# Kernel tuning notes

Measured on AMD Instinct MI355X. Metric: run time of the kernel, lower is better.

The kernel has to match this reference:

```python
import jax, jax.numpy as jnp
import numpy as np

B, S, IN, H, D, M, OUT, TOPK = 4, 256, 256, 512, 128, 100000, 256, 3
EPS = 1e-12  # F.normalize eps


def _l2norm(x):
    n = jnp.sqrt(jnp.sum(x * x, axis=-1, keepdims=True))
    return x / jnp.maximum(n, EPS)


def setup_inputs() -> dict:
    key = jax.random.key(0)
    ks = jax.random.split(key, 16)
    s = 0.02
    return {
        "x": jax.random.normal(ks[0], (B, S, IN), jnp.float32),
        # LSTM params (torch gate order i,f,g,o)
        "W_ih": jax.random.normal(ks[1], (4 * H, IN), jnp.float32) * s,
        "W_hh": jax.random.normal(ks[2], (4 * H, H), jnp.float32) * s,
        "b_ih": jax.random.normal(ks[3], (4 * H,), jnp.float32) * s,
        "b_hh": jax.random.normal(ks[4], (4 * H,), jnp.float32) * s,
        # memory interface
        "Wq": jax.random.normal(ks[5], (D, H), jnp.float32) * s,
        "bq": jax.random.normal(ks[6], (D,), jnp.float32) * s,
        "Wa": jax.random.normal(ks[7], (1, D), jnp.float32) * s,
        "ba": jax.random.normal(ks[8], (1,), jnp.float32) * s,
        "Wc": jax.random.normal(ks[9], (D, D), jnp.float32) * s,
        "bc": jax.random.normal(ks[10], (D,), jnp.float32) * s,
        # output layer
        "Wo": jax.random.normal(ks[11], (OUT, H + D), jnp.float32) * s,
        "bo": jax.random.normal(ks[12], (OUT,), jnp.float32) * s,
        # memory bank (importance_weight == 1.0 for all fresh entries)
        "mem_keys": jax.random.normal(ks[13], (M, D), jnp.float32),
        "mem_values": jax.random.normal(ks[14], (M, D), jnp.float32),
    }


def _lstm(x, W_ih, W_hh, b_ih, b_hh):
    b = b_ih + b_hh
    xg = jnp.einsum('bsi,gi->bsg', x, W_ih) + b  # (B,S,4H)

    def step(carry, xg_t):
        h, c = carry
        g = xg_t + h @ W_hh.T
        i, f, gg, o = jnp.split(g, 4, axis=-1)
        c = jax.nn.sigmoid(f) * c + jax.nn.sigmoid(i) * jnp.tanh(gg)
        h = jax.nn.sigmoid(o) * jnp.tanh(c)
        return (h, c), h

    h0 = jnp.zeros((x.shape[0], W_hh.shape[1]), x.dtype)
    (_, _), hs = jax.lax.scan(step, (h0, h0), jnp.swapaxes(xg, 0, 1))
    return jnp.swapaxes(hs, 0, 1)  # (B,S,H)


def reference(x, W_ih, W_hh, b_ih, b_hh, Wq, bq, Wa, ba, Wc, bc, Wo, bo, mem_keys, mem_values):
    h = _lstm(x, W_ih, W_hh, b_ih, b_hh)               # (B,S,H)
    q = _l2norm(h @ Wq.T + bq)                          # (B,S,D) normalized query
    kn = _l2norm(mem_keys)                              # (M,D)
    sims = jnp.einsum('bsd,md->bsm', q, kn)             # cosine sims (x1.0 importance)
    _, idx = jax.lax.top_k(sims, TOPK)                  # (B,S,K)
    retrieved = mem_values[idx]                         # (B,S,K,D) gather
    att = jax.nn.softmax(jnp.squeeze(retrieved @ Wa.T + ba, -1), axis=-1)  # (B,S,K)
    mem = jnp.einsum('bsk,bskd->bsd', att, retrieved)
    mem = mem @ Wc.T + bc                               # combine_layer
    out = jnp.concatenate([h, mem], axis=-1) @ Wo.T + bo  # (B,S,OUT)
    return out
```

## Files before the change

### kernel.cpp

```cpp
#include <hip/hip_runtime.h>
#include <math.h>

#define INF __builtin_inff()
#define SENT 0x7FA00000u
#define IMAX 0x7fffffff

typedef __attribute__((ext_vector_type(8))) short bhalf8;
typedef __attribute__((ext_vector_type(4))) float f32x4;


__device__ __forceinline__ void ins3b(float& v0, int& i0, float& v1, int& i1,
                                      float& v2, int& i2, float nv, int ni) {
  bool b0 = (nv > v0) || (nv == v0 && ni < i0);
  bool b1 = (nv > v1) || (nv == v1 && ni < i1);
  bool b2 = (nv > v2) || (nv == v2 && ni < i2);
  v2 = b1 ? v1 : (b2 ? nv : v2);
  i2 = b1 ? i1 : (b2 ? ni : i2);
  v1 = b0 ? v0 : (b1 ? nv : v1);
  i1 = b0 ? i0 : (b1 ? ni : i1);
  v0 = b0 ? nv : v0;
  i0 = b0 ? ni : i0;
}

__device__ __forceinline__ unsigned short f2bf(float x) {
  unsigned u = __float_as_uint(x);
  return (unsigned short)((u + 0x7FFFu + ((u >> 16) & 1u)) >> 16);
}

__global__ void init_k(float* __restrict__ base) {
  int t = blockIdx.x * 256 + threadIdx.x;
  if (t < 2623488) {
    bool zero = (t >= 2097152) && (t < 2097152 + 2048);
    base[t] = zero ? 0.f : __uint_as_float(SENT);
  }
}

template<int AMODE>
__global__ __launch_bounds__(256) void gemm_k(
    const float* __restrict__ A, const float* __restrict__ A2,
    const float* __restrict__ Bw, const float* __restrict__ b1,
    const float* __restrict__ b2, float* __restrict__ C,
    int M, int N, int K) {
  __shared__ float4 As4[64][16];
  __shared__ float4 Bs4[64][16];
  const int t = threadIdx.x;
  const int tx = t & 15, ty = t >> 4;
  const int brow = blockIdx.x * 64, bcol = blockIdx.y * 64;
  const int srow = t >> 2, scb = t & 3;
  float acc[4][4] = {};
  for (int kt = 0; kt < K; kt += 64) {
#pragma unroll
    for (int u = 0; u < 4; ++u) {
      int c = scb + 4 * u;
      int gk = kt + c * 4;
      int gr = brow + srow;
      const float* ap;
      if (AMODE == 0) {
        ap = A + (size_t)gr * K + gk;
      } else {
        int b = gr >> 8, s = gr & 255;
        const float* hrow = A + ((size_t)(s + 1) * 4 + b) * 512;
        if (AMODE == 1) ap = hrow + gk;
        else ap = (gk < 512) ? (hrow + gk) : (A2 + (size_t)gr * 128 + (gk - 512));
      }
      As4[srow][c ^ (srow & 15)] = *(const float4*)ap;
      Bs4[srow][c ^ (srow & 15)] = *(const float4*)(Bw + (size_t)(bcol + srow) * K + gk);
    }
    __syncthreads();
#pragma unroll
    for (int d4 = 0; d4 < 16; ++d4) {
      float4 av[4], bv[4];
#pragma unroll
      for (int i = 0; i < 4; ++i) av[i] = As4[ty * 4 + i][d4 ^ ((ty * 4 + i) & 15)];
#pragma unroll
      for (int j = 0; j < 4; ++j) bv[j] = Bs4[tx * 4 + j][d4 ^ ((tx * 4 + j) & 15)];
#pragma unroll
      for (int i = 0; i < 4; ++i)
#pragma unroll
        for (int j = 0; j < 4; ++j)
          acc[i][j] += av[i].x * bv[j].x + av[i].y * bv[j].y +
                       av[i].z * bv[j].z + av[i].w * bv[j].w;
    }
    __syncthreads();
  }
#pragma unroll
  for (int i = 0; i < 4; ++i) {
    int r = brow + ty * 4 + i;
#pragma unroll
    for (int j = 0; j < 4; ++j) {
      int n = bcol + tx * 4 + j;
      float bias = b1[n];
      if (b2) bias += b2[n];
      C[(size_t)r * N + n] = acc[i][j] + bias;
    }
  }
}

__global__ __launch_bounds__(512, 2) void fused_front(
    const float* __restrict__ x, const float* __restrict__ W_ih,
    const float* __restrict__ b_ih, const float* __restrict__ b_hh,
    const float* __restrict__ W_hh, const float* __restrict__ keys,
    float* __restrict__ xg, float* __restrict__ h_seq,
    float* __restrict__ invn, unsigned* __restrict__ kbf) {
  __shared__ alignas(16) unsigned char smem[32768];
  const int bid = blockIdx.x;
  const int t = threadIdx.x;

  if (bid < 64) {
    const int batch = bid >> 4;
    const int ub = bid & 15;
    const int uu = t >> 4;
    const int li = t & 15;
    const int unit = ub * 32 + uu;
    float* h_lds = (float*)smem;

    float w[4][32];
#pragma unroll
    for (int g = 0; g < 4; ++g) {
      const float* wr = W_hh + (size_t)(g * 512 + unit) * 512 + li * 32;
#pragma unroll
      for (int j = 0; j < 32; j += 4) {
        float4 v = *(const float4*)(wr + j);
        w[g][j] = v.x; w[g][j + 1] = v.y; w[g][j + 2] = v.z; w[g][j + 3] = v.w;
      }
    }
    float c = 0.f;
    float xgv[4];
    {
      float* xq = xg + (size_t)(batch * 256) * 2048 + unit;
      bool again;
      do {
        again = false;
#pragma unroll
        for (int g = 0; g < 4; ++g)
          xgv[g] = __hip_atomic_load(xq + g * 512, __ATOMIC_RELAXED,
                                     __HIP_MEMORY_SCOPE_AGENT);
#pragma unroll
        for (int g = 0; g < 4; ++g)
          again |= (__float_as_uint(xgv[g]) == SENT);
      } while (again);
    }

    for (int step = 0; step < 256; ++step) {
      {
        float* hp = h_seq + ((size_t)step * 4 + batch) * 512 + t;
        float hv;
        do {
          hv = __hip_atomic_load(hp, __ATOMIC_RELAXED, __HIP_MEMORY_SCOPE_AGENT);
        } while (__float_as_uint(hv) == SENT);
        h_lds[(step & 1) * 576 + (t >> 5) * 36 + (t & 31)] = hv;
      }
      __syncthreads();
      const float* hb = h_lds + (step & 1) * 576 + li * 36;
      float a0 = 0.f, a1 = 0.f, a2 = 0.f, a3 = 0.f;
#pragma unroll
      for (int j = 0; j < 32; j += 4) {
        float4 hv = *(const float4*)(hb + j);
        a0 += w[0][j] * hv.x + w[0][j + 1] * hv.y + w[0][j + 2] * hv.z + w[0][j + 3] * hv.w;
        a1 += w[1][j] * hv.x + w[1][j + 1] * hv.y + w[1][j + 2] * hv.z + w[1][j + 3] * hv.w;
        a2 += w[2][j] * hv.x + w[2][j + 1] * hv.y + w[2][j + 2] * hv.z + w[2][j + 3] * hv.w;
        a3 += w[3][j] * hv.x + w[3][j + 1] * hv.y + w[3][j + 2] * hv.z + w[3][j + 3] * hv.w;
      }
#pragma unroll
      for (int m = 1; m < 16; m <<= 1) {
        a0 += __shfl_xor(a0, m, 64); a1 += __shfl_xor(a1, m, 64);
        a2 += __shfl_xor(a2, m, 64); a3 += __shfl_xor(a3, m, 64);
      }
      a0 += xgv[0]; a1 += xgv[1]; a2 += xgv[2]; a3 += xgv[3];
      float i_ = 1.f / (1.f + expf(-a0));
      float f_ = 1.f / (1.f + expf(-a1));
      float g_ = tanhf(a2);
      float o_ = 1.f / (1.f + expf(-a3));
      c = f_ * c + i_ * g_;
      float h = o_ * tanhf(c);
      if (li == 0)
        __hip_atomic_store(h_seq + ((size_t)(step + 1) * 4 + batch) * 512 + unit,
                           h, __ATOMIC_RELAXED, __HIP_MEMORY_SCOPE_AGENT);
      if (step < 255) {
        float* xq = xg + (size_t)(batch * 256 + step + 1) * 2048 + unit;
        bool again;
        do {
          again = false;
#pragma unroll
          for (int g = 0; g < 4; ++g)
            xgv[g] = __hip_atomic_load(xq + g * 512, __ATOMIC_RELAXED,
                                       __HIP_MEMORY_SCOPE_AGENT);
#pragma unroll
          for (int g = 0; g < 4; ++g)
            again |= (__float_as_uint(xgv[g]) == SENT);
        } while (again);
      }
    }
  } else if (bid < 576) {
    const int g = bid - 64;
    const int q = g >> 7;
    const int b = (g >> 5) & 3;
    const int col = g & 31;
    const int brow = (b * 4 + q) * 64, bcol = col * 64;
    float4* As4 = (float4*)smem;
    float4* Bs4 = (float4*)(smem + 16384);
    const int tx = t & 15, ty = (t >> 4) & 15;
    const int srow = (t & 255) >> 2, scb = t & 3;
    float acc[4][4] = {};
    for (int kt = 0; kt < 256; kt += 64) {
      if (t < 256) {
#pragma unroll
        for (int u = 0; u < 4; ++u) {
          int cc = scb + 4 * u;
          int gk = kt + cc * 4;
          As4[srow * 16 + (cc ^ (srow & 15))] =
              *(const float4*)(x + (size_t)(brow + srow) * 256 + gk);
          Bs4[srow * 16 + (cc ^ (srow & 15))] =
              *(const float4*)(W_ih + (size_t)(bcol + srow) * 256 + gk);
        }
      }
      __syncthreads();
      if (t < 256) {
#pragma unroll
        for (int d4 = 0; d4 < 16; ++d4) {
          float4 av[4], bv[4];
#pragma unroll
          for (int i = 0; i < 4; ++i)
            av[i] = As4[(ty * 4 + i) * 16 + (d4 ^ ((ty * 4 + i) & 15))];
#pragma unroll
          for (int j = 0; j < 4; ++j)
            bv[j] = Bs4[(tx * 4 + j) * 16 + (d4 ^ ((tx * 4 + j) & 15))];
#pragma unroll
          for (int i = 0; i < 4; ++i)
#pragma unroll
            for (int j = 0; j < 4; ++j)
              acc[i][j] += av[i].x * bv[j].x + av[i].y * bv[j].y +
                           av[i].z * bv[j].z + av[i].w * bv[j].w;
        }
      }
      __syncthreads();
    }
    if (t < 256) {
#pragma unroll
      for (int i = 0; i < 4; ++i) {
        int r = brow + ty * 4 + i;
#pragma unroll
        for (int j = 0; j < 4; ++j) {
          int n = bcol + tx * 4 + j;
          __hip_atomic_store(xg + (size_t)r * 2048 + n,
                             acc[i][j] + b_ih[n] + b_hh[n],
                             __ATOMIC_RELAXED, __HIP_MEMORY_SCOPE_AGENT);
        }
      }
    }
  } else {
    const int rb = (bid - 576) * 256;
    const int wv = t >> 6, lane = t & 63;
    for (int p = 0; p < 32; ++p) {
      int r = rb + p * 8 + wv;
      if (r < 100000) {
        float2 v = *(const float2*)(keys + (size_t)r * 128 + lane * 2);
        float ss = v.x * v.x + v.y * v.y;
#pragma unroll
        for (int m = 1; m < 64; m <<= 1) ss += __shfl_xor(ss, m, 64);
        float inv = 1.f / fmaxf(sqrtf(ss), 1e-12f);
        if (lane == 0) invn[r] = inv;
        kbf[(size_t)r * 64 + lane] =
            (unsigned)f2bf(v.x * inv) | ((unsigned)f2bf(v.y * inv) << 16);
      }
    }
  }
}

__global__ __launch_bounds__(256) void qnorm_k(float* __restrict__ q,
                                               unsigned* __restrict__ qbf) {
  int wv = threadIdx.x >> 6, lane = threadIdx.x & 63;
  int r = blockIdx.x * 4 + wv;
  float2 v = *(float2*)(q + (size_t)r * 128 + lane * 2);
  float ss = v.x * v.x + v.y * v.y;
#pragma unroll
  for (int m = 1; m < 64; m <<= 1) ss += __shfl_xor(ss, m, 64);
  float inv = 1.f / fmaxf(sqrtf(ss), 1e-12f);
  v.x *= inv; v.y *= inv;
  *(float2*)(q + (size_t)r * 128 + lane * 2) = v;
  qbf[(size_t)r * 64 + lane] = (unsigned)f2bf(v.x) | ((unsigned)f2bf(v.y) << 16);
}

__device__ __forceinline__ void stage_tile(unsigned short* dst,
                                           const unsigned* src,
                                           int baserow, int maxrow,
                                           int w, int l) {
#pragma unroll
  for (int u = 0; u < 4; ++u) {
    int s = u * 256 + w * 64 + l;
    int row = s >> 4, cc = s & 15;
    int gr = baserow + row; gr = gr > maxrow ? maxrow : gr;
    const unsigned* sp = src + (size_t)gr * 64 + ((cc ^ (row & 7)) << 2);
    __builtin_amdgcn_global_load_lds(
        (const __attribute__((address_space(1))) unsigned*)sp,
        (__attribute__((address_space(3))) unsigned*)(dst + (size_t)(u * 256 + w * 64) * 8),
        16, 0, 0);
  }
}

__global__ __launch_bounds__(256, 2) void simsmfma_k(
    const unsigned* __restrict__ qbf, const unsigned* __restrict__ kbf,
    float* __restrict__ pvals, int* __restrict__ pidx) {
  const int qt = blockIdx.x, ch = blockIdx.y;
  const int kbeg = ch * 3125, klim = kbeg + 3125;
  const int t = threadIdx.x, l = t & 63, w = t >> 6;
  __shared__ alignas(16) unsigned short ks0[8192];
  __shared__ alignas(16) unsigned short ks1[8192];

  stage_tile(ks1, qbf, qt * 64, 1023, w, l);
  __syncthreads();
  bhalf8 afrag[4];
  {
    int row = w * 16 + (l & 15);
#pragma unroll
    for (int db = 0; db < 4; ++db) {
      int cslot = db * 4 + (l >> 4);
      afrag[db] = *(const bhalf8*)&ks1[(size_t)(row * 16 + (cslot ^ (row & 7))) * 8];
    }
  }
  stage_tile(ks0, kbf, kbeg, klim - 1, w, l);
  __syncthreads();

  float tv0[4], tv1[4], tv2[4]; int ti0[4], ti1[4], ti2[4];
#pragma unroll
  for (int r = 0; r < 4; ++r) {
    tv0[r] = tv1[r] = tv2[r] = -INF;
    ti0[r] = ti1[r] = ti2[r] = IMAX;
  }

  for (int s = 0; s < 49; ++s) {
    unsigned short* cur = (s & 1) ? ks1 : ks0;
    unsigned short* nxt = (s & 1) ? ks0 : ks1;
    if (s < 48) stage_tile(nxt, kbf, kbeg + (s + 1) * 64, klim - 1, w, l);
    int k0 = kbeg + s * 64;

    f32x4 ac0 = {0,0,0,0}, ac1 = {0,0,0,0}, ac2 = {0,0,0,0}, ac3 = {0,0,0,0};
    const int r0 = l & 15;
#pragma unroll
    for (int db = 0; db < 4; ++db) {
      int swz = (db * 4 + (l >> 4)) ^ (r0 & 7);
      bhalf8 b0 = *(const bhalf8*)&cur[(size_t)((r0     ) * 16 + swz) * 8];
      bhalf8 b1 = *(const bhalf8*)&cur[(size_t)((r0 + 16) * 16 + swz) * 8];
      bhalf8 b2 = *(const bhalf8*)&cur[(size_t)((r0 + 32) * 16 + swz) * 8];
      bhalf8 b3 = *(const bhalf8*)&cur[(size_t)((r0 + 48) * 16 + swz) * 8];
      ac0 = __builtin_amdgcn_mfma_f32_16x16x32_bf16(afrag[db], b0, ac0, 0, 0, 0);
      ac1 = __builtin_amdgcn_mfma_f32_16x16x32_bf16(afrag[db], b1, ac1, 0, 0, 0);
      ac2 = __builtin_amdgcn_mfma_f32_16x16x32_bf16(afrag[db], b2, ac2, 0, 0, 0);
      ac3 = __builtin_amdgcn_mfma_f32_16x16x32_bf16(afrag[db], b3, ac3, 0, 0, 0);
    }
#pragma unroll
    for (int nt = 0; nt < 4; ++nt) {
      f32x4 a = (nt == 0) ? ac0 : (nt == 1) ? ac1 : (nt == 2) ? ac2 : ac3;
      int gk = k0 + nt * 16 + (l & 15);
      bool ok = gk < klim;
#pragma unroll
      for (int r = 0; r < 4; ++r) {
        float v = ok ? a[r] : -INF;
        ins3b(tv0[r], ti0[r], tv1[r], ti1[r], tv2[r], ti2[r], v, gk);
      }
    }
    __syncthreads();
  }

#pragma unroll
  for (int r = 0; r < 4; ++r) {
    float c0 = tv0[r], c1 = tv1[r], c2 = tv2[r];
    int j0 = ti0[r], j1 = ti1[r], j2 = ti2[r];
    int qrow = qt * 64 + w * 16 + (l >> 4) * 4 + r;
    size_t ob = ((size_t)ch * 1024 + qrow) * 6;
#pragma unroll
    for (int e = 0; e < 6; ++e) {
      float mv = c0; int mi = j0;
#pragma unroll
      for (int m = 1; m < 16; m <<= 1) {
        float o = __shfl_xor(mv, m, 64); int oi = __shfl_xor(mi, m, 64);
        bool tk = (o > mv) || (o == mv && oi < mi);
        mv = tk ? o : mv; mi = tk ? oi : mi;
      }
      if (mi == j0) { c0 = c1; j0 = j1; c1 = c2; j1 = j2; c2 = -INF; j2 = IMAX; }
      if ((l & 15) == 0) { pvals[ob + e] = mv; pidx[ob + e] = mi; }
    }
  }
}

__global__ __launch_bounds__(256) void merge_rescore_k(
    const float* __restrict__ pvals, const int* __restrict__ pidx,
    const float* __restrict__ qf, const float* __restrict__ keys,
    const float* __restrict__ invn, const float* __restrict__ mvals,
    const float* __restrict__ Wa, const float* __restrict__ ba,
    float* __restrict__ mem_pre) {
  int wv = threadIdx.x >> 6, l = threadIdx.x & 63;
  int qr = blockIdx.x * 4 + wv;
  float h0 = -INF, h1 = -INF, h2 = -INF;
  int g0 = IMAX, g1 = IMAX, g2 = IMAX;
#pragma unroll
  for (int e = 0; e < 3; ++e) {
    int c = l * 3 + e;
    size_t base = ((size_t)(c / 6) * 1024 + qr) * 6 + (c % 6);
    ins3b(h0, g0, h1, g1, h2, g2, pvals[base], pidx[base]);
  }
  float sc[8]; int si[8];
#pragma unroll
  for (int e = 0; e < 8; ++e) {
    float mv = h0; int mi = g0;
#pragma unroll
    for (int m = 1; m < 64; m <<= 1) {
      float o = __shfl_xor(mv, m, 64); int oi = __shfl_xor(mi, m, 64);
      bool tk = (o > mv) || (o == mv && oi < mi);
      mv = tk ? o : mv; mi = tk ? oi : mi;
    }
    sc[e] = mv; si[e] = mi;
    if (mi == g0) { h0 = h1; g0 = g1; h1 = h2; g1 = g2; h2 = -INF; g2 = IMAX; }
  }
  int d = l * 2;
  float q0 = qf[(size_t)qr * 128 + d], q1 = qf[(size_t)qr * 128 + d + 1];
  float ex[8];
#pragma unroll
  for (int e = 0; e < 8; ++e) {
    int k = si[e];
    float p = q0 * keys[(size_t)k * 128 + d] + q1 * keys[(size_t)k * 128 + d + 1];
#pragma unroll
    for (int m = 1; m < 64; m <<= 1) p += __shfl_xor(p, m, 64);
    ex[e] = p * invn[k];
  }
  float v0 = -INF, v1 = -INF, v2 = -INF;
  int i0 = IMAX, i1 = IMAX, i2 = IMAX;
#pragma unroll
  for (int e = 0; e < 8; ++e) ins3b(v0, i0, v1, i1, v2, i2, ex[e], si[e]);
  float r00 = mvals[(size_t)i0 * 128 + d], r01 = mvals[(size_t)i0 * 128 + d + 1];
  float r10 = mvals[(size_t)i1 * 128 + d], r11 = mvals[(size_t)i1 * 128 + d + 1];
  float r20 = mvals[(size_t)i2 * 128 + d], r21 = mvals[(size_t)i2 * 128 + d + 1];
  float wa0 = Wa[d], wa1 = Wa[d + 1];
  float p0 = wa0 * r00 + wa1 * r01;
  float p1 = wa0 * r10 + wa1 * r11;
  float p2 = wa0 * r20 + wa1 * r21;
#pragma unroll
  for (int m = 1; m < 64; m <<= 1) {
    p0 += __shfl_xor(p0, m, 64);
    p1 += __shfl_xor(p1, m, 64);
    p2 += __shfl_xor(p2, m, 64);
  }
  float bav = ba[0];
  float l0 = p0 + bav, l1 = p1 + bav, l2 = p2 + bav;
  float mx = fmaxf(l0, fmaxf(l1, l2));
  float e0 = expf(l0 - mx), e1 = expf(l1 - mx), e2 = expf(l2 - mx);
  float s = e0 + e1 + e2;
  float a0 = e0 / s, a1 = e1 / s, a2 = e2 / s;
  mem_pre[(size_t)qr * 128 + d]     = a0 * r00 + a1 * r10 + a2 * r20;
  mem_pre[(size_t)qr * 128 + d + 1] = a0 * r01 + a1 * r11 + a2 * r21;
}

extern "C" void kernel_launch(void* const* d_in, const int* in_sizes, int n_in,
                              void* d_out, int out_size, void* d_ws, size_t ws_size,
                              hipStream_t stream) {
  (void)in_sizes; (void)n_in; (void)out_size; (void)ws_size;
  const float* x    = (const float*)d_in[0];
  const float* W_ih = (const float*)d_in[1];
  const float* W_hh = (const float*)d_in[2];
  const float* b_ih = (const float*)d_in[3];
  const float* b_hh = (const float*)d_in[4];
  const float* Wq   = (const float*)d_in[5];
  const float* bq   = (const float*)d_in[6];
  const float* Wa   = (const float*)d_in[7];
  const float* ba   = (const float*)d_in[8];
  const float* Wc   = (const float*)d_in[9];
  const float* bc   = (const float*)d_in[10];
  const float* Wo   = (const float*)d_in[11];
  const float* bo   = (const float*)d_in[12];
  const float* keys = (const float*)d_in[13];
  const float* vals = (const float*)d_in[14];

  float* ws      = (float*)d_ws;
  float* xg      = ws + 0;
  float* h_seq   = ws + 2097152;
  float* qbuf    = ws + 2623488;
  float* invn    = ws + 2754560;
  float* mem_pre = ws + 2854560;
  float* mem_cmb = ws + 2985632;
  float* pvals   = ws + 3116704;
  int*   pidx    = (int*)(ws + 3313312);
  unsigned* qbf  = (unsigned*)(ws + 3509920);
  unsigned* kbf  = (unsigned*)(ws + 3575456);

  init_k<<<10248, 256, 0, stream>>>(ws);
  fused_front<<<967, 512, 0, stream>>>(x, W_ih, b_ih, b_hh, W_hh, keys,
                                       xg, h_seq, invn, kbf);
  gemm_k<1><<<dim3(16, 2), 256, 0, stream>>>(h_seq, nullptr, Wq, bq, nullptr,
                                             qbuf, 1024, 128, 512);
  qnorm_k<<<256, 256, 0, stream>>>(qbuf, qbf);
  simsmfma_k<<<dim3(16, 32), 256, 0, stream>>>(qbf, kbf, pvals, pidx);
  merge_rescore_k<<<256, 256, 0, stream>>>(pvals, pidx, qbuf, keys, invn, vals,
                                           Wa, ba, mem_pre);
  gemm_k<0><<<dim3(16, 2), 256, 0, stream>>>(mem_pre, nullptr, Wc, bc, nullptr,
                                             mem_cmb, 1024, 128, 128);
  gemm_k<2><<<dim3(16, 4), 256, 0, stream>>>(h_seq, mem_cmb, Wo, bo, nullptr,
                                             (float*)d_out, 1024, 256, 640);
}
```

Measured before the change: 1.159 ms.

## Replace per-element xg sentinel polling with per-chunk ready counters and prefetch

The xg input-projection buffer is no longer pre-filled with sentinels and polled element by element. Each GEMM tile now bumps a per-(batch,64-step chunk) counter with release semantics, and the LSTM blocks wait on that counter once per 64 steps, then read xg with plain loads one step ahead. This shrinks the init kernel and takes atomic spin loads off the serial recurrence path. The flags reuse the pvals workspace, which is safe only if nothing reads pvals before simsmfma overwrites it.

```diff
diff --git a/kernel.cpp b/kernel.cpp
--- a/kernel.cpp
+++ b/kernel.cpp
@@ -27,12 +27,10 @@
   return (unsigned short)((u + 0x7FFFu + ((u >> 16) & 1u)) >> 16);
 }
 
-__global__ void init_k(float* __restrict__ base) {
+__global__ void init_k(float* __restrict__ h_seq, unsigned* __restrict__ flags) {
   int t = blockIdx.x * 256 + threadIdx.x;
-  if (t < 2623488) {
-    bool zero = (t >= 2097152) && (t < 2097152 + 2048);
-    base[t] = zero ? 0.f : __uint_as_float(SENT);
-  }
+  if (t < 526336) h_seq[t] = (t < 2048) ? 0.f : __uint_as_float(SENT);
+  if (t < 16) flags[t] = 0u;
 }
 
 template<int AMODE>
@@ -101,7 +99,8 @@
     const float* __restrict__ b_ih, const float* __restrict__ b_hh,
     const float* __restrict__ W_hh, const float* __restrict__ keys,
     float* __restrict__ xg, float* __restrict__ h_seq,
-    float* __restrict__ invn, unsigned* __restrict__ kbf) {
+    float* __restrict__ invn, unsigned* __restrict__ kbf,
+    unsigned* __restrict__ xgflag) {
   __shared__ alignas(16) unsigned char smem[32768];
   const int bid = blockIdx.x;
   const int t = threadIdx.x;
@@ -125,20 +124,18 @@
       }
     }
     float c = 0.f;
-    float xgv[4];
     {
-      float* xq = xg + (size_t)(batch * 256) * 2048 + unit;
-      bool again;
-      do {
-        again = false;
-#pragma unroll
-        for (int g = 0; g < 4; ++g)
-          xgv[g] = __hip_atomic_load(xq + g * 512, __ATOMIC_RELAXED,
-                                     __HIP_MEMORY_SCOPE_AGENT);
-#pragma unroll
-        for (int g = 0; g < 4; ++g)
-          again |= (__float_as_uint(xgv[g]) == SENT);
-      } while (again);
+      const unsigned* f0 = xgflag + batch * 4;
+      while (__hip_atomic_load(f0, __ATOMIC_RELAXED, __HIP_MEMORY_SCOPE_AGENT) < 32u) {}
+      (void)__hip_atomic_load(f0, __ATOMIC_ACQUIRE, __HIP_MEMORY_SCOPE_AGENT);
+    }
+    float xcur[4], xnxt[4];
+    {
+      const float* xq = xg + (size_t)(batch * 256) * 2048 + unit;
+#pragma unroll
+      for (int g = 0; g < 4; ++g) xcur[g] = xq[g * 512];
+#pragma unroll
+      for (int g = 0; g < 4; ++g) xnxt[g] = xq[2048 + g * 512];
     }
 
     for (int step = 0; step < 256; ++step) {
@@ -166,7 +163,7 @@
         a0 += __shfl_xor(a0, m, 64); a1 += __shfl_xor(a1, m, 64);
         a2 += __shfl_xor(a2, m, 64); a3 += __shfl_xor(a3, m, 64);
       }
-      a0 += xgv[0]; a1 += xgv[1]; a2 += xgv[2]; a3 += xgv[3];
+      a0 += xcur[0]; a1 += xcur[1]; a2 += xcur[2]; a3 += xcur[3];
       float i_ = 1.f / (1.f + expf(-a0));
       float f_ = 1.f / (1.f + expf(-a1));
       float g_ = tanhf(a2);
@@ -176,19 +173,17 @@
       if (li == 0)
         __hip_atomic_store(h_seq + ((size_t)(step + 1) * 4 + batch) * 512 + unit,
                            h, __ATOMIC_RELAXED, __HIP_MEMORY_SCOPE_AGENT);
-      if (step < 255) {
-        float* xq = xg + (size_t)(batch * 256 + step + 1) * 2048 + unit;
-        bool again;
-        do {
-          again = false;
-#pragma unroll
-          for (int g = 0; g < 4; ++g)
-            xgv[g] = __hip_atomic_load(xq + g * 512, __ATOMIC_RELAXED,
-                                       __HIP_MEMORY_SCOPE_AGENT);
-#pragma unroll
-          for (int g = 0; g < 4; ++g)
-            again |= (__float_as_uint(xgv[g]) == SENT);
-        } while (again);
+#pragma unroll
+      for (int g = 0; g < 4; ++g) xcur[g] = xnxt[g];
+      if (step + 2 < 256) {
+        if (((step + 2) & 63) == 0) {
+          const unsigned* fq = xgflag + batch * 4 + ((step + 2) >> 6);
+          while (__hip_atomic_load(fq, __ATOMIC_RELAXED, __HIP_MEMORY_SCOPE_AGENT) < 32u) {}
+          (void)__hip_atomic_load(fq, __ATOMIC_ACQUIRE, __HIP_MEMORY_SCOPE_AGENT);
+        }
+        const float* xq = xg + (size_t)(batch * 256 + step + 2) * 2048 + unit;
+#pragma unroll
+        for (int g = 0; g < 4; ++g) xnxt[g] = xq[g * 512];
       }
     }
   } else if (bid < 576) {
@@ -242,12 +237,14 @@
 #pragma unroll
         for (int j = 0; j < 4; ++j) {
           int n = bcol + tx * 4 + j;
-          __hip_atomic_store(xg + (size_t)r * 2048 + n,
-                             acc[i][j] + b_ih[n] + b_hh[n],
-                             __ATOMIC_RELAXED, __HIP_MEMORY_SCOPE_AGENT);
+          xg[(size_t)r * 2048 + n] = acc[i][j] + b_ih[n] + b_hh[n];
         }
       }
     }
+    __syncthreads();
+    if (t == 0)
+      __hip_atomic_fetch_add(xgflag + b * 4 + q, 1u, __ATOMIC_RELEASE,
+                             __HIP_MEMORY_SCOPE_AGENT);
   } else {
     const int rb = (bid - 576) * 256;
     const int wv = t >> 6, lane = t & 63;
@@ -481,10 +478,11 @@
   int*   pidx    = (int*)(ws + 3313312);
   unsigned* qbf  = (unsigned*)(ws + 3509920);
   unsigned* kbf  = (unsigned*)(ws + 3575456);
-
-  init_k<<<10248, 256, 0, stream>>>(ws);
+  unsigned* xgflag = (unsigned*)pvals;
+
+  init_k<<<2056, 256, 0, stream>>>(h_seq, xgflag);
   fused_front<<<967, 512, 0, stream>>>(x, W_ih, b_ih, b_hh, W_hh, keys,
-                                       xg, h_seq, invn, kbf);
+                                       xg, h_seq, invn, kbf, xgflag);
   gemm_k<1><<<dim3(16, 2), 256, 0, stream>>>(h_seq, nullptr, Wq, bq, nullptr,
                                              qbuf, 1024, 128, 512);
   qnorm_k<<<256, 256, 0, stream>>>(qbuf, qbf);
```

Result: faster. 1.133 ms (-2.2%).
